# Optimization experiments

Measured on AMD Instinct MI355X. Metric: run time of the kernel, lower is better.

Reference implementation:

```python
import jax, jax.numpy as jnp
import numpy as np

B, C, L = 8, 512, 2048   # batch, input_dim (channels), sequence length
H = 8                    # multihead_cnt
K = 3                    # kernel_dim
DH = C // H              # per-head dim = 64
SCALE = 1.0 / float(np.sqrt(C))  # module divides by sqrt(input_dim), not sqrt(head_dim)


def _conv1d(x, w, b):
    # x: [B, C, L], w: [C_out, C_in, K], padding=1 keeps L
    y = jax.lax.conv_general_dilated(x, w, window_strides=(1,), padding=[(1, 1)],
                                     dimension_numbers=('NCH', 'OIH', 'NCH'))
    return y + b[None, :, None]


def setup_inputs() -> dict:
    key = jax.random.key(0)
    ks = jax.random.split(key, 7)
    x = jax.random.normal(ks[0], (B, C, L), dtype=jnp.float32)
    # xavier_normal_ std for Conv1d weight [C, C, K]: sqrt(2 / (fan_in + fan_out)), fan = C*K
    std = float(np.sqrt(2.0 / (C * K + C * K)))
    inp = {'x': x}
    for i in range(3):  # conv_cnt = 3 -> q, k, v convolutions
        inp[f'w{i}'] = jax.random.normal(ks[1 + 2 * i], (C, C, K), dtype=jnp.float32) * std
        inp[f'b{i}'] = jax.random.normal(ks[2 + 2 * i], (C,), dtype=jnp.float32) * 0.01
    return inp


def reference(x, w0, b0, w1, b1, w2, b2):
    # q, k, v projections via Conv1d (padding preserves length)
    q = _conv1d(x, w0, b0)  # [B, C, L]
    k = _conv1d(x, w1, b1)
    v = _conv1d(x, w2, b2)
    # torch.chunk along dim 1 == contiguous reshape into heads
    qh = q.reshape(B, H, DH, L)
    kh = k.reshape(B, H, DH, L)
    vh = v.reshape(B, H, DH, L)
    # scores = q^T k / sqrt(input_dim)  -> [B, H, L, L]
    scores = jnp.einsum('bhdl,bhdm->bhlm', qh, kh) * SCALE
    att = jax.nn.softmax(scores, axis=-1)
    # out = (att @ v^T)^T -> [B, H, DH, L]
    out = jnp.einsum('bhlm,bhdm->bhdl', att, vh)
    return out.reshape(B, C, L)
```

## Files before the change

### kernel.cpp

```cpp
#include <hip/hip_runtime.h>
#include <hip/hip_bf16.h>
#include <cstdint>

typedef unsigned short u16;
typedef short v8s __attribute__((ext_vector_type(8)));
typedef float v4f __attribute__((ext_vector_type(4)));
typedef u16 u16x8 __attribute__((ext_vector_type(8)));
typedef u16 u16x4 __attribute__((ext_vector_type(4)));

static constexpr int Bb = 8, Cc = 512, Ll = 2048, Hh = 8, Dh = 64;

__device__ __forceinline__ float bf2f(u16 u){
  unsigned x = ((unsigned)u) << 16; float f; __builtin_memcpy(&f, &x, 4); return f;
}
__device__ __forceinline__ u16 f2bf(float f){
  unsigned x; __builtin_memcpy(&x, &f, 4);
  x = (x + 0x7fffu + ((x >> 16) & 1u)) >> 16; return (u16)x;
}

__device__ __forceinline__ void async_cp16(const u16* g, u16* l){
  __builtin_amdgcn_global_load_lds(
      (const __attribute__((address_space(1))) unsigned int*)g,
      (__attribute__((address_space(3))) unsigned int*)l, 16, 0, 0);
}

#if __has_builtin(__builtin_amdgcn_exp2f)
#define EXP2F(x) __builtin_amdgcn_exp2f(x)
#else
#define EXP2F(x) exp2f(x)
#endif

__global__ __launch_bounds__(256) void detect_dtype(const u16* __restrict__ x, unsigned* __restrict__ flag){
  __shared__ int cnt;
  if (threadIdx.x == 0) cnt = 0;
  __syncthreads();
  int sane = 0;
  for (int i = threadIdx.x; i < 4096; i += 256){
    unsigned e = (x[2 * i] >> 7) & 0xFFu;
    sane += (e >= 90u && e <= 160u) ? 1 : 0;
  }
  atomicAdd(&cnt, sane);
  __syncthreads();
  if (threadIdx.x == 0) *flag = (cnt < 2458) ? 1u : 0u;
}

__global__ __launch_bounds__(256) void transpose_pad(const void* __restrict__ xv, const unsigned* __restrict__ flagp,
                                                     u16* __restrict__ xT){
  int b = blockIdx.z, ci0 = blockIdx.y * 64, l0 = blockIdx.x * 64;
  __shared__ u16 tb[64 * 72];
  const unsigned isf32 = *flagp;
  int t = threadIdx.x;
  int row = t >> 3, seg = t & 7;
  if (isf32){
    const float* xf = (const float*)xv;
    #pragma unroll
    for (int rnd = 0; rnd < 2; rnd++){
      int ci = row + rnd * 32;
      size_t off = ((size_t)(b * Cc + ci0 + ci)) * Ll + l0 + seg * 8;
      v4f a = *(const v4f*)(xf + off);
      v4f c4 = *(const v4f*)(xf + off + 4);
      #pragma unroll
      for (int j = 0; j < 4; j++) tb[(seg * 8 + j) * 72 + ci] = f2bf(a[j]);
      #pragma unroll
      for (int j = 0; j < 4; j++) tb[(seg * 8 + 4 + j) * 72 + ci] = f2bf(c4[j]);
    }
  } else {
    const u16* x = (const u16*)xv;
    #pragma unroll
    for (int rnd = 0; rnd < 2; rnd++){
      int ci = row + rnd * 32;
      u16x8 v = *(const u16x8*)(x + ((size_t)(b * Cc + ci0 + ci)) * Ll + l0 + seg * 8);
      #pragma unroll
      for (int j = 0; j < 8; j++) tb[(seg * 8 + j) * 72 + ci] = v[j];
    }
  }
  __syncthreads();
  #pragma unroll
  for (int rnd = 0; rnd < 2; rnd++){
    int l = row + rnd * 32;
    u16x8 v = *(const u16x8*)&tb[l * 72 + seg * 8];
    *(u16x8*)(xT + ((size_t)b * 2050 + 1 + l0 + l) * Cc + ci0 + seg * 8) = v;
  }
  if (blockIdx.x == 0 && t < 8){
    u16x8 z = {};
    *(u16x8*)(xT + ((size_t)b * 2050 + 0) * Cc + ci0 + t * 8) = z;
  }
  if (blockIdx.x == 31 && t < 8){
    u16x8 z = {};
    *(u16x8*)(xT + ((size_t)b * 2050 + 2049) * Cc + ci0 + t * 8) = z;
  }
}

__global__ __launch_bounds__(256) void pack_wb(const void* __restrict__ w0, const void* __restrict__ w1,
                                               const void* __restrict__ w2, const void* __restrict__ b0,
                                               const void* __restrict__ b1, const void* __restrict__ b2,
                                               const unsigned* __restrict__ flagp,
                                               u16* __restrict__ wp, u16* __restrict__ bb){
  int g = blockIdx.x * 256 + threadIdx.x;
  const unsigned isf32 = *flagp;
  if (g < 9 * 512 * 512){
    int ci = g & 511, co = (g >> 9) & 511, kc = g >> 18;
    int conv = kc / 3, k = kc - conv * 3;
    const void* w = (conv == 0) ? w0 : ((conv == 1) ? w1 : w2);
    size_t idx = (size_t)co * 1536 + ci * 3 + k;
    wp[g] = isf32 ? f2bf(((const float*)w)[idx]) : ((const u16*)w)[idx];
  } else {
    int g2 = g - 9 * 512 * 512;
    if (g2 < 1536){
      int conv = g2 >> 9, c = g2 & 511;
      const void* bsrc = (conv == 0) ? b0 : ((conv == 1) ? b1 : b2);
      bb[g2] = isf32 ? f2bf(((const float*)bsrc)[c]) : ((const u16*)bsrc)[c];
    }
  }
}

__global__ __launch_bounds__(512, 2) void conv_gemm_fused(const u16* __restrict__ wp, const u16* __restrict__ xT,
                                                          const u16* __restrict__ bb, u16* __restrict__ qT,
                                                          u16* __restrict__ kT, u16* __restrict__ vN){
  __shared__ u16 smem[73728];
  int bx = blockIdx.x;
  int b = bx & 7, inner = bx >> 3;
  int mt = inner >> 3, nt = inner & 7;
  int m0 = mt << 7, n0 = nt << 8;
  int conv = m0 >> 9, co0 = m0 & 511;

  int t = threadIdx.x, wave = t >> 6, lane = t & 63, quad = lane >> 4, lid = lane & 15;
  int wm_i = wave >> 2, wn_i = wave & 3;

  int sx = (lid & 7) << 4;
  int cb0 = ((quad * 16) ^ sx) >> 1;
  int cb1 = ((64 + quad * 16) ^ sx) >> 1;
  int abase0 = (wm_i * 64 + lid) * 64;
  int bbase0 = 8192 + (wn_i * 64 + lid) * 64;

  int srcA[2], srcB[4];
  #pragma unroll
  for (int r = 0; r < 2; r++){
    int p = t * 16 + r * 8192;
    int row = p >> 7, c = (p & 127) ^ ((row & 7) << 4);
    srcA[r] = row * 512 + (c >> 1);
  }
  #pragma unroll
  for (int r = 0; r < 4; r++){
    int p = t * 16 + r * 8192;
    int row = p >> 7, c = (p & 127) ^ ((row & 7) << 4);
    srcB[r] = row * 512 + (c >> 1);
  }
  int dA0 = t * 8, dA1 = t * 8 + 4096;

  const u16* aGbase = wp + (size_t)(conv * 1536 + co0) * 512;
  const u16* bGbase = xT + (size_t)b * (2050 * 512) + (size_t)n0 * 512;

#define STAGE_TILE(aG, bG, stg) do{ \
    async_cp16((aG) + srcA[0], (stg) + dA0); \
    async_cp16((aG) + srcA[1], (stg) + dA1); \
    _Pragma("unroll") for (int r = 0; r < 4; ++r) \
      async_cp16((bG) + srcB[r], (stg) + 8192 + t * 8 + r * 4096); }while(0)

#define LOAD_A() do{ \
    _Pragma("unroll") for (int m = 0; m < 4; ++m){ \
      af[m][0] = *(const v8s*)(lds + abase0 + m * 1024 + cb0); \
      af[m][1] = *(const v8s*)(lds + abase0 + m * 1024 + cb1); } }while(0)

#define LOAD_Bn(n) do{ \
    bfc[0] = *(const v8s*)(lds + bbase0 + (n) * 1024 + cb0); \
    bfc[1] = *(const v8s*)(lds + bbase0 + (n) * 1024 + cb1); }while(0)

#define MFMA_COL(n) do{ \
    __builtin_amdgcn_s_setprio(1); \
    _Pragma("unroll") for (int m = 0; m < 4; ++m) \
    _Pragma("unroll") for (int kh = 0; kh < 2; ++kh) \
      acc[m][n] = __builtin_amdgcn_mfma_f32_16x16x32_bf16(af[m][kh], bfc[kh], acc[m][n], 0, 0, 0); \
    __builtin_amdgcn_s_setprio(0); }while(0)

  v4f acc[4][4] = {};
  v8s af[4][2], bfc[2];

  STAGE_TILE(aGbase, bGbase, smem);
  STAGE_TILE(aGbase + 64, bGbase + 64, smem + 24576);
  asm volatile("s_waitcnt vmcnt(6)" ::: "memory");
  __builtin_amdgcn_sched_barrier(0);
  __builtin_amdgcn_s_barrier();

  #pragma unroll 3
  for (int kt = 0; kt < 24; ++kt){
    u16* lds = smem + (kt % 3) * 24576;
    if (kt < 22){
      int k2 = kt + 2;
      int ks2 = k2 >> 3, ci2 = (k2 & 7) << 6;
      const u16* aG = aGbase + (size_t)ks2 * 262144 + ci2;
      const u16* bG = bGbase + (size_t)ks2 * 512 + ci2;
      u16* stg = smem + (k2 % 3) * 24576;
      STAGE_TILE(aG, bG, stg);
    }
    LOAD_A();
    LOAD_Bn(0); MFMA_COL(0);
    LOAD_Bn(1); MFMA_COL(1);
    LOAD_Bn(2); MFMA_COL(2);
    LOAD_Bn(3); MFMA_COL(3);
    if (kt < 22){
      asm volatile("s_waitcnt vmcnt(6)" ::: "memory");
      __builtin_amdgcn_sched_barrier(0);
      __builtin_amdgcn_s_barrier();
    } else if (kt == 22){
      asm volatile("s_waitcnt vmcnt(0)" ::: "memory");
      __builtin_amdgcn_sched_barrier(0);
      __builtin_amdgcn_s_barrier();
    }
  }

#undef STAGE_TILE
#undef LOAD_A
#undef LOAD_Bn
#undef MFMA_COL

  const float qsc = (float)(1.4426950408889634 / 22.627416997969522);
  if (conv < 2){
    u16* dst = (conv == 0) ? qT : kT;
    #pragma unroll
    for (int m = 0; m < 4; ++m){
      int cog = m0 + wm_i * 64 + m * 16 + quad * 4;
      float bv[4];
      #pragma unroll
      for (int r = 0; r < 4; r++) bv[r] = bf2f(bb[cog + r]);
      int coc = cog & 511;
      #pragma unroll
      for (int n = 0; n < 4; ++n){
        int l = n0 + wn_i * 64 + n * 16 + lid;
        u16x4 pk;
        #pragma unroll
        for (int r = 0; r < 4; r++){
          float v = acc[m][n][r] + bv[r];
          if (conv == 0) v *= qsc;
          pk[r] = f2bf(v);
        }
        *(u16x4*)(dst + ((((size_t)b * Hh + (coc >> 6)) * Ll + l) << 6) + (coc & 63)) = pk;
      }
    }
  } else {
    u16* scr = smem;
    __syncthreads();
    #pragma unroll
    for (int m = 0; m < 4; ++m){
      int rloc = wm_i * 64 + m * 16 + quad * 4;
      int cog = m0 + rloc;
      float bv[4];
      #pragma unroll
      for (int r = 0; r < 4; r++) bv[r] = bf2f(bb[cog + r]);
      #pragma unroll
      for (int n = 0; n < 4; ++n){
        int lcl = wn_i * 64 + n * 16 + lid;
        #pragma unroll
        for (int r = 0; r < 4; r++)
          scr[(rloc + r) * 264 + lcl] = f2bf(acc[m][n][r] + bv[r]);
      }
    }
    __syncthreads();
    int seg = t & 31, rw = t >> 5;
    #pragma unroll
    for (int ps = 0; ps < 8; ++ps){
      int row = rw + ps * 16;
      u16x8 vv = *(const u16x8*)&scr[row * 264 + seg * 8];
      *(u16x8*)(vN + (((size_t)b * Cc + co0 + row) << 11) + n0 + seg * 8) = vv;
    }
  }
}

__global__ __launch_bounds__(512) void attn_kernel(const u16* __restrict__ qT, const u16* __restrict__ kT,
                                                   const u16* __restrict__ vN, const unsigned* __restrict__ flagp,
                                                   void* __restrict__ outv){
  int bhx = blockIdx.x;
  int b = bhx >> 3, h = bhx & 7, l0 = blockIdx.y * 256;
  int t = threadIdx.x, w = t >> 6, lane = t & 63, quad = lane >> 4, lid = lane & 15;
  __shared__ u16 kls[2][8192];
  __shared__ u16 vls[2][8192];
  const unsigned isf32 = *flagp;
  const size_t bh = (size_t)b * Hh + h;
  const int xk = (lid & 7) << 3;

  int kadd[2], vadd[2];
  #pragma unroll
  for (int r = 0; r < 2; r++){
    int e = (r * 512 + t) * 8;
    int slot = e >> 6, col = e & 63;
    int s5 = slot & 31;
    int m = (slot & ~31) | (((s5 >> 2) & 1) << 3) | (((s5 >> 3) & 1) << 4) | (((s5 >> 4) & 1) << 2) | (s5 & 3);
    kadd[r] = m * 64 + (col ^ ((slot & 7) << 3));
    int half = e >> 12, d = (e >> 6) & 63;
    vadd[r] = d * Ll + half * 64 + (col ^ ((d & 7) << 3));
  }
  const u16* kTb = kT + bh * Ll * 64;
  const u16* vNb = vN + ((size_t)(b * Cc + h * Dh)) * Ll;

#define STAGE_KV(mt1) do{ \
    const u16* kp = kTb + (size_t)(mt1) * 8192; \
    const u16* vp = vNb + (mt1) * 128; \
    u16* kd = &kls[(mt1) & 1][0]; \
    u16* vd = &vls[(mt1) & 1][0]; \
    async_cp16(kp + kadd[0], kd + t * 8); \
    async_cp16(kp + kadd[1], kd + 4096 + t * 8); \
    async_cp16(vp + vadd[0], vd + t * 8); \
    async_cp16(vp + vadd[1], vd + 4096 + t * 8); }while(0)

  v8s qF[2][2];
  #pragma unroll
  for (int ci = 0; ci < 2; ci++)
    #pragma unroll
    for (int ks = 0; ks < 2; ks++)
      qF[ci][ks] = *(const v8s*)(qT + ((bh * Ll) + l0 + w * 32 + ci * 16 + lid) * 64 + ks * 32 + quad * 8);
  __builtin_amdgcn_sched_barrier(0);

  const v8s onesF = {0x3F80, 0x3F80, 0x3F80, 0x3F80, 0x3F80, 0x3F80, 0x3F80, 0x3F80};
  v4f o[2][4] = {};
  v4f o1[2] = {};

  STAGE_KV(0);
  asm volatile("s_waitcnt vmcnt(2)" ::: "memory");
  __builtin_amdgcn_sched_barrier(0);
  __builtin_amdgcn_s_barrier();

  for (int mt = 0; mt < 16; mt++){
    if (mt < 15) STAGE_KV(mt + 1);
    const u16* kcur = &kls[mt & 1][0];
    const u16* vcur = &vls[mt & 1][0];

    v4f s[4][2][2] = {};
    #pragma unroll
    for (int ks = 0; ks < 2; ks++){
      v8s aF[4][2];
      #pragma unroll
      for (int c = 0; c < 4; c++)
        #pragma unroll
        for (int tt = 0; tt < 2; tt++)
          aF[c][tt] = *(const v8s*)&kcur[(c * 32 + tt * 16 + lid) * 64 + ((ks * 32 + quad * 8) ^ xk)];
      __builtin_amdgcn_s_setprio(1);
      #pragma unroll
      for (int c = 0; c < 4; c++)
        #pragma unroll
        for (int tt = 0; tt < 2; tt++){
          s[c][tt][0] = __builtin_amdgcn_mfma_f32_16x16x32_bf16(aF[c][tt], qF[0][ks], s[c][tt][0], 0, 0, 0);
          s[c][tt][1] = __builtin_amdgcn_mfma_f32_16x16x32_bf16(aF[c][tt], qF[1][ks], s[c][tt][1], 0, 0, 0);
        }
      __builtin_amdgcn_s_setprio(0);
    }

    if (mt < 15){
      asm volatile("s_waitcnt vmcnt(4)" ::: "memory");
    } else {
      asm volatile("s_waitcnt vmcnt(0)" ::: "memory");
    }
    __builtin_amdgcn_sched_barrier(0);
    __builtin_amdgcn_s_barrier();

    #pragma unroll
    for (int c = 0; c < 4; c++){
      v8s aP[2];
      #pragma unroll
      for (int ci = 0; ci < 2; ci++){
        float p[8];
        #pragma unroll
        for (int tt = 0; tt < 2; tt++)
          #pragma unroll
          for (int r = 0; r < 4; r++)
            p[tt * 4 + r] = EXP2F(s[c][tt][ci][r]);
        unsigned u[4];
        #pragma unroll
        for (int k2 = 0; k2 < 4; k2++){
          __hip_bfloat162 hb = __float22bfloat162_rn(make_float2(p[2 * k2], p[2 * k2 + 1]));
          __builtin_memcpy(&u[k2], &hb, 4);
        }
        __builtin_memcpy(&aP[ci], u, 16);
      }
      v8s bV[4];
      #pragma unroll
      for (int df = 0; df < 4; df++)
        bV[df] = *(const v8s*)&vcur[(c >> 1) * 4096 + (df * 16 + lid) * 64 + ((((c & 1) * 32) + quad * 8) ^ xk)];
      __builtin_amdgcn_s_setprio(1);
      #pragma unroll
      for (int ci = 0; ci < 2; ci++){
        #pragma unroll
        for (int df = 0; df < 4; df++)
          o[ci][df] = __builtin_amdgcn_mfma_f32_16x16x32_bf16(aP[ci], bV[df], o[ci][df], 0, 0, 0);
        o1[ci] = __builtin_amdgcn_mfma_f32_16x16x32_bf16(aP[ci], onesF, o1[ci], 0, 0, 0);
      }
      __builtin_amdgcn_s_setprio(0);
    }

    if (mt < 15){
      asm volatile("s_waitcnt vmcnt(2)" ::: "memory");
      __builtin_amdgcn_sched_barrier(0);
      __builtin_amdgcn_s_barrier();
    }
  }
#undef STAGE_KV

  #pragma unroll
  for (int lf = 0; lf < 2; lf++){
    v4f nv;
    #pragma unroll
    for (int r = 0; r < 4; r++) nv[r] = 1.f / o1[lf][r];
    #pragma unroll
    for (int df = 0; df < 4; df++){
      int d = df * 16 + lid;
      int l = l0 + w * 32 + lf * 16 + quad * 4;
      size_t ofs = (((bh << 6) + d) << 11) + l;
      if (isf32){
        v4f st;
        #pragma unroll
        for (int r = 0; r < 4; r++) st[r] = o[lf][df][r] * nv[r];
        *(v4f*)((float*)outv + ofs) = st;
      } else {
        u16x4 pk;
        #pragma unroll
        for (int r = 0; r < 4; r++) pk[r] = f2bf(o[lf][df][r] * nv[r]);
        *(u16x4*)((u16*)outv + ofs) = pk;
      }
    }
  }
}

extern "C" void kernel_launch(void* const* d_in, const int* in_sizes, int n_in,
                              void* d_out, int out_size, void* d_ws, size_t ws_size,
                              hipStream_t stream){
  const void* x  = d_in[0];
  const void* w0 = d_in[1];
  const void* b0 = d_in[2];
  const void* w1 = d_in[3];
  const void* b1 = d_in[4];
  const void* w2 = d_in[5];
  const void* b2 = d_in[6];
  u16* ws = (u16*)d_ws;
  unsigned* flag = (unsigned*)ws;
  u16* xT = ws + 64;
  u16* wp = xT + (size_t)8 * 2050 * 512;
  u16* bb = wp + (size_t)9 * 512 * 512;
  u16* qT = bb + 1536;
  u16* kT = qT + (size_t)8 * 8 * 2048 * 64;
  u16* vN = kT + (size_t)8 * 8 * 2048 * 64;

  detect_dtype<<<1, 256, 0, stream>>>((const u16*)x, flag);
  transpose_pad<<<dim3(32, 8, 8), 256, 0, stream>>>(x, flag, xT);
  pack_wb<<<dim3(9 * 512 * 512 / 256 + 6), 256, 0, stream>>>(w0, w1, w2, b0, b1, b2, flag, wp, bb);
  conv_gemm_fused<<<dim3(768), 512, 0, stream>>>(wp, xT, bb, qT, kT, vN);
  attn_kernel<<<dim3(64, 8), 512, 0, stream>>>(qT, kT, vN, flag, d_out);
}
```

Before: 272.9 us.

## Load conv GEMM weight tiles directly into registers, staging only activations in LDS

The fused QKV conv GEMM stops staging the weight (A) tile through shared memory. Each wave now loads its A fragments straight from global memory into registers, using two ping-pong register sets so the next k-step's weights are fetched while the current one computes. Only the activation (B) tile still goes through the triple-buffered LDS ring, so the LDS footprint shrinks from 144 KB to 96 KB. This removes the LDS write and read traffic for A, at the cost of more live registers and per-lane strided global loads, and the wait on outstanding memory operations now also covers the A prefetch.

```diff
diff --git a/kernel.cpp b/kernel.cpp
--- a/kernel.cpp
+++ b/kernel.cpp
@@ -117,7 +117,7 @@
 __global__ __launch_bounds__(512, 2) void conv_gemm_fused(const u16* __restrict__ wp, const u16* __restrict__ xT,
                                                           const u16* __restrict__ bb, u16* __restrict__ qT,
                                                           u16* __restrict__ kT, u16* __restrict__ vN){
-  __shared__ u16 smem[73728];
+  __shared__ u16 smem[49152];
   int bx = blockIdx.x;
   int b = bx & 7, inner = bx >> 3;
   int mt = inner >> 3, nt = inner & 7;
@@ -130,89 +130,87 @@
   int sx = (lid & 7) << 4;
   int cb0 = ((quad * 16) ^ sx) >> 1;
   int cb1 = ((64 + quad * 16) ^ sx) >> 1;
-  int abase0 = (wm_i * 64 + lid) * 64;
-  int bbase0 = 8192 + (wn_i * 64 + lid) * 64;
-
-  int srcA[2], srcB[4];
-  #pragma unroll
-  for (int r = 0; r < 2; r++){
-    int p = t * 16 + r * 8192;
-    int row = p >> 7, c = (p & 127) ^ ((row & 7) << 4);
-    srcA[r] = row * 512 + (c >> 1);
-  }
+  int bbase0 = (wn_i * 64 + lid) * 64;
+
+  int srcB[4];
   #pragma unroll
   for (int r = 0; r < 4; r++){
     int p = t * 16 + r * 8192;
     int row = p >> 7, c = (p & 127) ^ ((row & 7) << 4);
     srcB[r] = row * 512 + (c >> 1);
   }
-  int dA0 = t * 8, dA1 = t * 8 + 4096;
 
   const u16* aGbase = wp + (size_t)(conv * 1536 + co0) * 512;
   const u16* bGbase = xT + (size_t)b * (2050 * 512) + (size_t)n0 * 512;
-
-#define STAGE_TILE(aG, bG, stg) do{ \
-    async_cp16((aG) + srcA[0], (stg) + dA0); \
-    async_cp16((aG) + srcA[1], (stg) + dA1); \
+  const int arow = (wm_i * 64 + lid) * 512 + quad * 8;
+
+#define LOAD_AG(dst, k1) do{ \
+    int ks1_ = (k1) >> 3, ci1_ = ((k1) & 7) << 6; \
+    const u16* aG_ = aGbase + (size_t)ks1_ * 262144 + ci1_ + arow; \
+    _Pragma("unroll") for (int m = 0; m < 4; ++m){ \
+      dst[m][0] = *(const v8s*)(aG_ + m * 8192); \
+      dst[m][1] = *(const v8s*)(aG_ + m * 8192 + 32); } }while(0)
+
+#define STAGE_B(k2) do{ \
+    int ks2_ = (k2) >> 3, ci2_ = ((k2) & 7) << 6; \
+    const u16* bG_ = bGbase + (size_t)ks2_ * 512 + ci2_; \
+    u16* stg_ = smem + ((k2) % 3) * 16384; \
     _Pragma("unroll") for (int r = 0; r < 4; ++r) \
-      async_cp16((bG) + srcB[r], (stg) + 8192 + t * 8 + r * 4096); }while(0)
-
-#define LOAD_A() do{ \
-    _Pragma("unroll") for (int m = 0; m < 4; ++m){ \
-      af[m][0] = *(const v8s*)(lds + abase0 + m * 1024 + cb0); \
-      af[m][1] = *(const v8s*)(lds + abase0 + m * 1024 + cb1); } }while(0)
+      async_cp16(bG_ + srcB[r], stg_ + t * 8 + r * 4096); }while(0)
 
 #define LOAD_Bn(n) do{ \
     bfc[0] = *(const v8s*)(lds + bbase0 + (n) * 1024 + cb0); \
     bfc[1] = *(const v8s*)(lds + bbase0 + (n) * 1024 + cb1); }while(0)
 
-#define MFMA_COL(n) do{ \
+#define MFMA_COL(AC, n) do{ \
     __builtin_amdgcn_s_setprio(1); \
     _Pragma("unroll") for (int m = 0; m < 4; ++m) \
     _Pragma("unroll") for (int kh = 0; kh < 2; ++kh) \
-      acc[m][n] = __builtin_amdgcn_mfma_f32_16x16x32_bf16(af[m][kh], bfc[kh], acc[m][n], 0, 0, 0); \
+      acc[m][n] = __builtin_amdgcn_mfma_f32_16x16x32_bf16(AC[m][kh], bfc[kh], acc[m][n], 0, 0, 0); \
     __builtin_amdgcn_s_setprio(0); }while(0)
 
+#define KT_BODY(AC, AN, kt) do{ \
+    u16* lds = smem + ((kt) % 3) * 16384; \
+    if ((kt) < 23) LOAD_AG(AN, (kt) + 1); \
+    __builtin_amdgcn_sched_barrier(0); \
+    if ((kt) < 22) STAGE_B((kt) + 2); \
+    __builtin_amdgcn_sched_barrier(0); \
+    v8s bfc[2]; \
+    LOAD_Bn(0); MFMA_COL(AC, 0); \
+    LOAD_Bn(1); MFMA_COL(AC, 1); \
+    LOAD_Bn(2); MFMA_COL(AC, 2); \
+    LOAD_Bn(3); MFMA_COL(AC, 3); \
+    if ((kt) < 22){ \
+      asm volatile("s_waitcnt vmcnt(4)" ::: "memory"); \
+      __builtin_amdgcn_sched_barrier(0); \
+      __builtin_amdgcn_s_barrier(); \
+    } else if ((kt) == 22){ \
+      asm volatile("s_waitcnt vmcnt(0)" ::: "memory"); \
+      __builtin_amdgcn_sched_barrier(0); \
+      __builtin_amdgcn_s_barrier(); \
+    } }while(0)
+
   v4f acc[4][4] = {};
-  v8s af[4][2], bfc[2];
-
-  STAGE_TILE(aGbase, bGbase, smem);
-  STAGE_TILE(aGbase + 64, bGbase + 64, smem + 24576);
-  asm volatile("s_waitcnt vmcnt(6)" ::: "memory");
+  v8s afP[4][2], afQ[4][2];
+
+  LOAD_AG(afP, 0);
+  __builtin_amdgcn_sched_barrier(0);
+  STAGE_B(0);
+  STAGE_B(1);
+  asm volatile("s_waitcnt vmcnt(4)" ::: "memory");
   __builtin_amdgcn_sched_barrier(0);
   __builtin_amdgcn_s_barrier();
 
-  #pragma unroll 3
-  for (int kt = 0; kt < 24; ++kt){
-    u16* lds = smem + (kt % 3) * 24576;
-    if (kt < 22){
-      int k2 = kt + 2;
-      int ks2 = k2 >> 3, ci2 = (k2 & 7) << 6;
-      const u16* aG = aGbase + (size_t)ks2 * 262144 + ci2;
-      const u16* bG = bGbase + (size_t)ks2 * 512 + ci2;
-      u16* stg = smem + (k2 % 3) * 24576;
-      STAGE_TILE(aG, bG, stg);
-    }
-    LOAD_A();
-    LOAD_Bn(0); MFMA_COL(0);
-    LOAD_Bn(1); MFMA_COL(1);
-    LOAD_Bn(2); MFMA_COL(2);
-    LOAD_Bn(3); MFMA_COL(3);
-    if (kt < 22){
-      asm volatile("s_waitcnt vmcnt(6)" ::: "memory");
-      __builtin_amdgcn_sched_barrier(0);
-      __builtin_amdgcn_s_barrier();
-    } else if (kt == 22){
-      asm volatile("s_waitcnt vmcnt(0)" ::: "memory");
-      __builtin_amdgcn_sched_barrier(0);
-      __builtin_amdgcn_s_barrier();
-    }
-  }
-
-#undef STAGE_TILE
-#undef LOAD_A
+  for (int kt2 = 0; kt2 < 24; kt2 += 2){
+    KT_BODY(afP, afQ, kt2);
+    KT_BODY(afQ, afP, kt2 + 1);
+  }
+
+#undef LOAD_AG
+#undef STAGE_B
 #undef LOAD_Bn
 #undef MFMA_COL
+#undef KT_BODY
 
   const float qsc = (float)(1.4426950408889634 / 22.627416997969522);
   if (conv < 2){
```

Measured after the change: 370.6 us. +35.8%, slower.

## Shrink conv GEMM tile to 128x128 with 256 threads and double buffering

Applied to the files above, without the earlier changes.

Halves the conv-GEMM block tile along L, from 128x256 to 128x128. Blocks now have 4 waves in a 2x2 layout instead of 8, and twice as many blocks are launched. The LDS pipeline goes from a triple buffer with prefetch distance 2 to a double buffer with prefetch distance 1, which cuts LDS per block and should allow more blocks per CU. The trade-off is less operand reuse per block and less latency hiding, since each step now waits for all loads (vmcnt(0)) before its barrier.

```diff
diff --git a/kernel.cpp b/kernel.cpp
--- a/kernel.cpp
+++ b/kernel.cpp
@@ -114,18 +114,18 @@
   }
 }
 
-__global__ __launch_bounds__(512, 2) void conv_gemm_fused(const u16* __restrict__ wp, const u16* __restrict__ xT,
-                                                          const u16* __restrict__ bb, u16* __restrict__ qT,
-                                                          u16* __restrict__ kT, u16* __restrict__ vN){
-  __shared__ u16 smem[73728];
+__global__ __launch_bounds__(256) void conv_gemm_fused(const u16* __restrict__ wp, const u16* __restrict__ xT,
+                                                       const u16* __restrict__ bb, u16* __restrict__ qT,
+                                                       u16* __restrict__ kT, u16* __restrict__ vN){
+  __shared__ u16 smem[32768];
   int bx = blockIdx.x;
   int b = bx & 7, inner = bx >> 3;
-  int mt = inner >> 3, nt = inner & 7;
-  int m0 = mt << 7, n0 = nt << 8;
+  int mt = inner >> 4, nt = inner & 15;
+  int m0 = mt << 7, n0 = nt << 7;
   int conv = m0 >> 9, co0 = m0 & 511;
 
   int t = threadIdx.x, wave = t >> 6, lane = t & 63, quad = lane >> 4, lid = lane & 15;
-  int wm_i = wave >> 2, wn_i = wave & 3;
+  int wm_i = wave >> 1, wn_i = wave & 1;
 
   int sx = (lid & 7) << 4;
   int cb0 = ((quad * 16) ^ sx) >> 1;
@@ -133,29 +133,22 @@
   int abase0 = (wm_i * 64 + lid) * 64;
   int bbase0 = 8192 + (wn_i * 64 + lid) * 64;
 
-  int srcA[2], srcB[4];
-  #pragma unroll
-  for (int r = 0; r < 2; r++){
-    int p = t * 16 + r * 8192;
-    int row = p >> 7, c = (p & 127) ^ ((row & 7) << 4);
-    srcA[r] = row * 512 + (c >> 1);
-  }
+  int src[4];
   #pragma unroll
   for (int r = 0; r < 4; r++){
-    int p = t * 16 + r * 8192;
+    int p = t * 16 + r * 4096;
     int row = p >> 7, c = (p & 127) ^ ((row & 7) << 4);
-    srcB[r] = row * 512 + (c >> 1);
-  }
-  int dA0 = t * 8, dA1 = t * 8 + 4096;
+    src[r] = row * 512 + (c >> 1);
+  }
 
   const u16* aGbase = wp + (size_t)(conv * 1536 + co0) * 512;
   const u16* bGbase = xT + (size_t)b * (2050 * 512) + (size_t)n0 * 512;
 
 #define STAGE_TILE(aG, bG, stg) do{ \
-    async_cp16((aG) + srcA[0], (stg) + dA0); \
-    async_cp16((aG) + srcA[1], (stg) + dA1); \
     _Pragma("unroll") for (int r = 0; r < 4; ++r) \
-      async_cp16((bG) + srcB[r], (stg) + 8192 + t * 8 + r * 4096); }while(0)
+      async_cp16((aG) + src[r], (stg) + t * 8 + r * 2048); \
+    _Pragma("unroll") for (int r = 0; r < 4; ++r) \
+      async_cp16((bG) + src[r], (stg) + 8192 + t * 8 + r * 2048); }while(0)
 
 #define LOAD_A() do{ \
     _Pragma("unroll") for (int m = 0; m < 4; ++m){ \
@@ -177,20 +170,19 @@
   v8s af[4][2], bfc[2];
 
   STAGE_TILE(aGbase, bGbase, smem);
-  STAGE_TILE(aGbase + 64, bGbase + 64, smem + 24576);
-  asm volatile("s_waitcnt vmcnt(6)" ::: "memory");
+  asm volatile("s_waitcnt vmcnt(0)" ::: "memory");
   __builtin_amdgcn_sched_barrier(0);
   __builtin_amdgcn_s_barrier();
 
-  #pragma unroll 3
+  #pragma unroll 2
   for (int kt = 0; kt < 24; ++kt){
-    u16* lds = smem + (kt % 3) * 24576;
-    if (kt < 22){
-      int k2 = kt + 2;
-      int ks2 = k2 >> 3, ci2 = (k2 & 7) << 6;
-      const u16* aG = aGbase + (size_t)ks2 * 262144 + ci2;
-      const u16* bG = bGbase + (size_t)ks2 * 512 + ci2;
-      u16* stg = smem + (k2 % 3) * 24576;
+    u16* lds = smem + (kt & 1) * 16384;
+    u16* stg = smem + ((kt + 1) & 1) * 16384;
+    if (kt < 23){
+      int k1 = kt + 1;
+      int ks1 = k1 >> 3, ci1 = (k1 & 7) << 6;
+      const u16* aG = aGbase + (size_t)ks1 * 262144 + ci1;
+      const u16* bG = bGbase + (size_t)ks1 * 512 + ci1;
       STAGE_TILE(aG, bG, stg);
     }
     LOAD_A();
@@ -198,11 +190,7 @@
     LOAD_Bn(1); MFMA_COL(1);
     LOAD_Bn(2); MFMA_COL(2);
     LOAD_Bn(3); MFMA_COL(3);
-    if (kt < 22){
-      asm volatile("s_waitcnt vmcnt(6)" ::: "memory");
-      __builtin_amdgcn_sched_barrier(0);
-      __builtin_amdgcn_s_barrier();
-    } else if (kt == 22){
+    if (kt < 23){
       asm volatile("s_waitcnt vmcnt(0)" ::: "memory");
       __builtin_amdgcn_sched_barrier(0);
       __builtin_amdgcn_s_barrier();
@@ -252,15 +240,15 @@
         int lcl = wn_i * 64 + n * 16 + lid;
         #pragma unroll
         for (int r = 0; r < 4; r++)
-          scr[(rloc + r) * 264 + lcl] = f2bf(acc[m][n][r] + bv[r]);
+          scr[(rloc + r) * 132 + lcl] = f2bf(acc[m][n][r] + bv[r]);
       }
     }
     __syncthreads();
-    int seg = t & 31, rw = t >> 5;
+    int seg = t & 15, rw = t >> 4;
     #pragma unroll
     for (int ps = 0; ps < 8; ++ps){
       int row = rw + ps * 16;
-      u16x8 vv = *(const u16x8*)&scr[row * 264 + seg * 8];
+      u16x8 vv = *(const u16x8*)&scr[row * 132 + seg * 8];
       *(u16x8*)(vN + (((size_t)b * Cc + co0 + row) << 11) + n0 + seg * 8) = vv;
     }
   }
@@ -441,6 +429,6 @@
   detect_dtype<<<1, 256, 0, stream>>>((const u16*)x, flag);
   transpose_pad<<<dim3(32, 8, 8), 256, 0, stream>>>(x, flag, xT);
   pack_wb<<<dim3(9 * 512 * 512 / 256 + 6), 256, 0, stream>>>(w0, w1, w2, b0, b1, b2, flag, wp, bb);
-  conv_gemm_fused<<<dim3(768), 512, 0, stream>>>(wp, xT, bb, qT, kT, vN);
+  conv_gemm_fused<<<dim3(1536), 256, 0, stream>>>(wp, xT, bb, qT, kT, vN);
   attn_kernel<<<dim3(64, 8), 512, 0, stream>>>(qT, kT, vN, flag, d_out);
 }
```

Measured after the change: 269.9 us. Within noise of the previous version (-1.1%).

## Software-pipeline LDS fragment reads with MFMAs in conv GEMM main loop

Applied to the files above, without the earlier changes.

Restructures the conv-projection GEMM K-loop so that LDS reads of the next B column and of the next k-tile's A fragments are issued while the current column's MFMAs run. A and B fragments are double-buffered in registers, with explicit lgkmcnt waits. The goal is to hide LDS read latency behind matrix math. The cost is more VGPRs, which may lower occupancy, and an extra barrier per iteration.

```diff
diff --git a/kernel.cpp b/kernel.cpp
--- a/kernel.cpp
+++ b/kernel.cpp
@@ -157,62 +157,69 @@
     _Pragma("unroll") for (int r = 0; r < 4; ++r) \
       async_cp16((bG) + srcB[r], (stg) + 8192 + t * 8 + r * 4096); }while(0)
 
-#define LOAD_A() do{ \
+#define READ_A(dst, L) do{ \
     _Pragma("unroll") for (int m = 0; m < 4; ++m){ \
-      af[m][0] = *(const v8s*)(lds + abase0 + m * 1024 + cb0); \
-      af[m][1] = *(const v8s*)(lds + abase0 + m * 1024 + cb1); } }while(0)
-
-#define LOAD_Bn(n) do{ \
-    bfc[0] = *(const v8s*)(lds + bbase0 + (n) * 1024 + cb0); \
-    bfc[1] = *(const v8s*)(lds + bbase0 + (n) * 1024 + cb1); }while(0)
-
-#define MFMA_COL(n) do{ \
+      dst[m][0] = *(const v8s*)((L) + abase0 + m * 1024 + cb0); \
+      dst[m][1] = *(const v8s*)((L) + abase0 + m * 1024 + cb1); } }while(0)
+
+#define READ_B(dst, L, n) do{ \
+    dst[0] = *(const v8s*)((L) + bbase0 + (n) * 1024 + cb0); \
+    dst[1] = *(const v8s*)((L) + bbase0 + (n) * 1024 + cb1); }while(0)
+
+#define MFMA_COL(AC, BV, n) do{ \
     __builtin_amdgcn_s_setprio(1); \
     _Pragma("unroll") for (int m = 0; m < 4; ++m) \
     _Pragma("unroll") for (int kh = 0; kh < 2; ++kh) \
-      acc[m][n] = __builtin_amdgcn_mfma_f32_16x16x32_bf16(af[m][kh], bfc[kh], acc[m][n], 0, 0, 0); \
+      acc[m][n] = __builtin_amdgcn_mfma_f32_16x16x32_bf16(AC[m][kh], BV[kh], acc[m][n], 0, 0, 0); \
     __builtin_amdgcn_s_setprio(0); }while(0)
 
+#define LGKM0 do{ asm volatile("s_waitcnt lgkmcnt(0)" ::: "memory"); \
+    __builtin_amdgcn_sched_barrier(0); }while(0)
+
+#define KT_BODY(AC, AN, kt) do{ \
+    u16* lds  = smem + ((kt) % 3) * 24576; \
+    u16* lds1 = smem + (((kt) + 1) % 3) * 24576; \
+    __builtin_amdgcn_s_barrier();                         \
+    if ((kt) <= 21){ \
+      int k2 = (kt) + 2, ks2 = k2 >> 3, ci2 = (k2 & 7) << 6; \
+      STAGE_TILE(aGbase + (size_t)ks2 * 262144 + ci2, bGbase + (size_t)ks2 * 512 + ci2, \
+                 smem + (k2 % 3) * 24576); \
+      asm volatile("s_waitcnt vmcnt(6)" ::: "memory");    \
+    } else if ((kt) == 22){ \
+      asm volatile("s_waitcnt vmcnt(0)" ::: "memory"); \
+    } \
+    __builtin_amdgcn_sched_barrier(0); \
+    __builtin_amdgcn_s_barrier();                         \
+    READ_B(bfB, lds, 1);  MFMA_COL(AC, bfA, 0);  LGKM0; \
+    READ_B(bfA, lds, 2);  MFMA_COL(AC, bfB, 1);  LGKM0; \
+    READ_B(bfB, lds, 3);  MFMA_COL(AC, bfA, 2);  LGKM0; \
+    if ((kt) < 23){ READ_A(AN, lds1); READ_B(bfA, lds1, 0); } \
+    MFMA_COL(AC, bfB, 3);  LGKM0; \
+  }while(0)
+
   v4f acc[4][4] = {};
-  v8s af[4][2], bfc[2];
+  v8s afP[4][2], afQ[4][2], bfA[2], bfB[2];
 
   STAGE_TILE(aGbase, bGbase, smem);
   STAGE_TILE(aGbase + 64, bGbase + 64, smem + 24576);
   asm volatile("s_waitcnt vmcnt(6)" ::: "memory");
   __builtin_amdgcn_sched_barrier(0);
   __builtin_amdgcn_s_barrier();
-
-  #pragma unroll 3
-  for (int kt = 0; kt < 24; ++kt){
-    u16* lds = smem + (kt % 3) * 24576;
-    if (kt < 22){
-      int k2 = kt + 2;
-      int ks2 = k2 >> 3, ci2 = (k2 & 7) << 6;
-      const u16* aG = aGbase + (size_t)ks2 * 262144 + ci2;
-      const u16* bG = bGbase + (size_t)ks2 * 512 + ci2;
-      u16* stg = smem + (k2 % 3) * 24576;
-      STAGE_TILE(aG, bG, stg);
-    }
-    LOAD_A();
-    LOAD_Bn(0); MFMA_COL(0);
-    LOAD_Bn(1); MFMA_COL(1);
-    LOAD_Bn(2); MFMA_COL(2);
-    LOAD_Bn(3); MFMA_COL(3);
-    if (kt < 22){
-      asm volatile("s_waitcnt vmcnt(6)" ::: "memory");
-      __builtin_amdgcn_sched_barrier(0);
-      __builtin_amdgcn_s_barrier();
-    } else if (kt == 22){
-      asm volatile("s_waitcnt vmcnt(0)" ::: "memory");
-      __builtin_amdgcn_sched_barrier(0);
-      __builtin_amdgcn_s_barrier();
-    }
+  READ_A(afP, smem);
+  READ_B(bfA, smem, 0);
+  LGKM0;
+
+  for (int kp = 0; kp < 24; kp += 2){
+    KT_BODY(afP, afQ, kp);
+    KT_BODY(afQ, afP, kp + 1);
   }
 
 #undef STAGE_TILE
-#undef LOAD_A
-#undef LOAD_Bn
+#undef READ_A
+#undef READ_B
 #undef MFMA_COL
+#undef LGKM0
+#undef KT_BODY
 
   const float qsc = (float)(1.4426950408889634 / 22.627416997969522);
   if (conv < 2){
```

Result: no change. 276.2 us (+1.2%).
